# Kernel optimization log

Measured on AMD Instinct MI355X. Metric: run time of the kernel, lower is better.

Reference implementation:

```python
import jax, jax.numpy as jnp
import numpy as np

B, C, H, W, K = 8, 512, 64, 64, 3
EPS = 1e-8


def setup_inputs() -> dict:
    key = jax.random.key(0)
    ks = jax.random.split(key, 7)
    return {
        "x": jax.random.normal(ks[0], (B, C, H, W), jnp.float32),
        "w": jax.random.normal(ks[1], (B, C), jnp.float32),
        "noise": jax.random.normal(ks[2], (B, 1, H, W), jnp.float32),
        # learned params (randn init as in the torch module)
        "conv_weight": jax.random.normal(ks[3], (C, C, K, K), jnp.float32),   # [out_ch, in_ch, k, k]
        "style_weight": jax.random.normal(ks[4], (C, C), jnp.float32),        # EqualizedLinear weight
        "style_bias": jnp.zeros((C,), jnp.float32),
        "bias": jax.random.normal(ks[5], (C,), jnp.float32),
        "scale_noise": jax.random.normal(ks[6], (1,), jnp.float32),
    }


def reference(x, w, noise, conv_weight, style_weight, style_bias, bias, scale_noise):
    b, c, h, wd = x.shape
    c_style = 1.0 / np.sqrt(C)          # EqualizedWeights c for [C, C]
    c_conv = 1.0 / np.sqrt(C * K * K)   # EqualizedWeights c for [C, C, K, K]

    # style vector s: equalized linear
    s = w @ (style_weight * c_style).T + style_bias            # [B, C]

    # per-sample modulation of input channels, demodulation per output channel
    wmod = (conv_weight * c_conv)[None] * s[:, None, :, None, None]   # [B, O, I, K, K]
    demod = jax.lax.rsqrt(jnp.sum(wmod * wmod, axis=(2, 3, 4), keepdims=True) + EPS)
    wmod = wmod * demod

    # grouped conv: fold batch into channels, one group per sample
    xg = x.reshape(1, b * c, h, wd)
    wg = wmod.reshape(b * C, C, K, K)
    y = jax.lax.conv_general_dilated(
        xg, wg, window_strides=(1, 1), padding="SAME",
        feature_group_count=b, dimension_numbers=("NCHW", "OIHW", "NCHW"))
    y = y.reshape(b, C, h, wd)

    # noise + bias + LeakyReLU(0.2)
    y = y + scale_noise[None, :, None, None] * noise
    return jax.nn.leaky_relu(y + bias[None, :, None, None], negative_slope=0.2)
```

## Files before the change

### kernel.cpp

```cpp
#include <hip/hip_runtime.h>


#define CC 512
#define BB 8
#define HWSZ 4096

#define C_STYLE 0.04419417382415922f
#define C_CONV  0.014731391274719739f

typedef __attribute__((ext_vector_type(8))) short bf16x8;
typedef __attribute__((ext_vector_type(4))) float f32x4;

static __device__ __forceinline__ short f2bf(float f) {
  unsigned u = __float_as_uint(f);
  unsigned r = (u + 0x7fffu + ((u >> 16) & 1u)) >> 16;
  return (short)r;
}

static __device__ __forceinline__ void load_lds_16(const void* g, void* l) {
  __builtin_amdgcn_global_load_lds(
      (const __attribute__((address_space(1))) unsigned int*)g,
      (__attribute__((address_space(3))) unsigned int*)l, 16, 0, 0);
}

__global__ void wprep_kernel(const float* __restrict__ cw,
                             short* __restrict__ wfrag,
                             float* __restrict__ wsq) {
  int t0 = blockIdx.x * blockDim.x + threadIdx.x;
  int o = t0 >> 9;
  int i = t0 & 511;
  int ib32 = i >> 5;
  int ob = o >> 4;
  int lane = (o & 15) + (((i >> 3) & 3) << 4);
  int j = i & 7;
  const float* p = cw + (size_t)t0 * 9;
  float s = 0.f;
#pragma unroll
  for (int t = 0; t < 9; ++t) {
    float v = p[t];
    s = fmaf(v, v, s);
    wfrag[((((size_t)t * 16 + ib32) * 32 + ob) * 64 + lane) * 8 + j] = f2bf(v);
  }
  wsq[t0] = s;
}

__global__ void style_alpha_kernel(const float* __restrict__ w,
                                   const float* __restrict__ sw,
                                   const float* __restrict__ sbias,
                                   float* __restrict__ alpha) {
  int wv = (blockIdx.x * blockDim.x + threadIdx.x) >> 6;
  int lane = threadIdx.x & 63;
  int b = wv >> 9;
  int j = wv & 511;
  float acc = 0.f;
  const float* wr = w + b * CC;
  const float* sr = sw + (size_t)j * CC;
#pragma unroll
  for (int k = 0; k < CC; k += 64) acc = fmaf(wr[k + lane], sr[k + lane], acc);
#pragma unroll
  for (int off = 32; off > 0; off >>= 1) acc += __shfl_down(acc, off);
  if (lane == 0) alpha[wv] = C_CONV * fmaf(C_STYLE, acc, sbias[j]);
}

__global__ void demod_kernel(const float* __restrict__ alpha,
                             const float* __restrict__ wsq,
                             float* __restrict__ demod) {
  int wv = (blockIdx.x * blockDim.x + threadIdx.x) >> 6;
  int lane = threadIdx.x & 63;
  int b = wv >> 9;
  int o = wv & 511;
  const float* ar = alpha + b * CC;
  const float* qr = wsq + (size_t)o * CC;
  float s = 0.f;
#pragma unroll
  for (int i = 0; i < CC; i += 64) {
    float a = ar[i + lane];
    s = fmaf(a * a, qr[i + lane], s);
  }
#pragma unroll
  for (int off = 32; off > 0; off >>= 1) s += __shfl_down(s, off);
  if (lane == 0) {
    s += 1e-8f;
    float r = rsqrtf(s);
    r = r * fmaf(-0.5f * s * r, r, 1.5f);
    demod[wv] = r;
  }
}

__global__ void xprep_kernel(const float* __restrict__ x,
                             const float* __restrict__ alpha,
                             short* __restrict__ xT) {
  const int py = blockIdx.x;
  const int ic = blockIdx.y * 4 + (threadIdx.x >> 6);
  const int b = blockIdx.z;
  const int px = threadIdx.x & 63;
  bf16x8 v = (bf16x8){0, 0, 0, 0, 0, 0, 0, 0};
  if (py >= 1 && py <= 64) {
    const float* xp = x + (((size_t)b * CC + ic * 8) * HWSZ + (py - 1) * 64 + px);
    const float* al = alpha + b * CC + ic * 8;
#pragma unroll
    for (int j = 0; j < 8; ++j) v[j] = f2bf(xp[(size_t)j * HWSZ] * al[j]);
  }
  short* row = xT + (((size_t)(b * 64 + ic) * 66 + py) * 66) * 8;
  *(bf16x8*)(row + (px + 1) * 8) = v;
  bf16x8 z = (bf16x8){0, 0, 0, 0, 0, 0, 0, 0};
  if (px == 0) *(bf16x8*)(row) = z;
  if (px == 63) *(bf16x8*)(row + 65 * 8) = z;
}

#define NCHUNK 2112
__global__ __launch_bounds__(256, 2) void conv_kernel(
    const short* __restrict__ xT,
    const short* __restrict__ wfrag,
    const float* __restrict__ noise,
    const float* __restrict__ bias,
    const float* __restrict__ scale_noise,
    const float* __restrict__ demod,
    float* __restrict__ out) {
  __shared__ __align__(16) short xs[2 * NCHUNK * 8];

  const int lin = blockIdx.x + 32 * blockIdx.y + 64 * blockIdx.z;
  const int xcd = lin & 7;
  const int j = lin >> 3;
  const int G = xcd & 1;
  const int b = (xcd >> 1) + 4 * (j & 1);
  const int y0 = (j >> 1) * 2;
  const int tid = threadIdx.x;
  const int lane = tid & 63;
  const int wave = tid >> 6;
  const int n = lane & 15;
  const int quad = lane >> 4;

  f32x4 acc[4][8];
#pragma unroll
  for (int p = 0; p < 4; ++p)
#pragma unroll
    for (int q = 0; q < 8; ++q) acc[p][q] = (f32x4){0.f, 0.f, 0.f, 0.f};

  const char* xTb = (const char*)xT;
  unsigned goff[9];
#pragma unroll
  for (int it = 0; it < 9; ++it) {
    int cid = tid + it * 256;
    int kc = cid / 264;
    int rem = cid - kc * 264;
    int r = rem / 66;
    int c = rem - r * 66;
    goff[it] = (unsigned)((((b * 64 + kc) * 66 + (y0 + r)) * 66 + c) * 16);
  }

  const short* wf0 = wfrag + ((size_t)((G * 16 + wave * 4) * 64 + lane)) * 8;

#pragma unroll
  for (int it = 0; it < 9; ++it) {
    int cid = tid + it * 256;
    if (cid < NCHUNK) load_lds_16(xTb + goff[it], xs + (size_t)cid * 8);
    goff[it] += 8 * 66 * 66 * 16;
  }

  for (int ib = 0; ib < 8; ++ib) {
    const int sel = ib & 1;
    asm volatile("s_waitcnt vmcnt(0)" ::: "memory");
    __builtin_amdgcn_s_barrier();
    if (ib < 7) {
#pragma unroll
      for (int it = 0; it < 9; ++it) {
        int cid = tid + it * 256;
        if (cid < NCHUNK)
          load_lds_16(xTb + goff[it],
                      xs + (size_t)((sel ^ 1) * NCHUNK + cid) * 8);
        goff[it] += 8 * 66 * 66 * 16;
      }
    }
    const short* cxs = xs + (size_t)sel * NCHUNK * 8;

#pragma unroll
    for (int kstep = 0; kstep < 2; ++kstep) {
      const int ib32 = ib * 2 + kstep;
#pragma unroll
      for (int t = 0; t < 9; ++t) {
        const int dy = t / 3 - 1;
        const int dx = t % 3 - 1;
        const short* wp = wf0 + (size_t)(t * 16 + ib32) * 16384;
        bf16x8 af[4];
#pragma unroll
        for (int p = 0; p < 4; ++p)
          af[p] = *(const bf16x8*)(wp + p * 512);
        const short* bp =
            cxs + (((kstep * 4 + quad) * 4 + dy + 1) * 66 + 1 + n + dx) * 8;
        bf16x8 bf[8];
#pragma unroll
        for (int q = 0; q < 8; ++q)
          bf[q] = *(const bf16x8*)(bp + ((q >> 2) * 66 + (q & 3) * 16) * 8);
        __builtin_amdgcn_s_setprio(1);
#pragma unroll
        for (int p = 0; p < 4; ++p)
#pragma unroll
          for (int q = 0; q < 8; ++q)
            acc[p][q] = __builtin_amdgcn_mfma_f32_16x16x32_bf16(
                af[p], bf[q], acc[p][q], 0, 0, 0);
        __builtin_amdgcn_s_setprio(0);
      }
    }
  }

  const float sn = scale_noise[0];
#pragma unroll
  for (int q = 0; q < 8; ++q) {
    const int y = y0 + (q >> 2);
    const int col = (q & 3) * 16 + n;
    const float nz = sn * noise[b * HWSZ + y * 64 + col];
#pragma unroll
    for (int p = 0; p < 4; ++p) {
      const int o0 = G * 256 + wave * 64 + p * 16 + quad * 4;
#pragma unroll
      for (int r = 0; r < 4; ++r) {
        const int o = o0 + r;
        float v = fmaf(acc[p][q][r], demod[b * CC + o], nz + bias[o]);
        out[((size_t)(b * CC + o)) * HWSZ + y * 64 + col] =
            v > 0.f ? v : 0.2f * v;
      }
    }
  }
}

extern "C" void kernel_launch(void* const* d_in, const int* in_sizes, int n_in,
                              void* d_out, int out_size, void* d_ws, size_t ws_size,
                              hipStream_t stream) {
  const float* x     = (const float*)d_in[0];
  const float* w     = (const float*)d_in[1];
  const float* noise = (const float*)d_in[2];
  const float* cw    = (const float*)d_in[3];
  const float* sw    = (const float*)d_in[4];
  const float* sbias = (const float*)d_in[5];
  const float* bias  = (const float*)d_in[6];
  const float* sn    = (const float*)d_in[7];
  float* out = (float*)d_out;

  float* alpha = (float*)d_ws;
  float* demod = alpha + BB * CC;
  float* wsq   = demod + BB * CC;
  short* wfrag = (short*)(wsq + CC * CC);
  short* xT    = wfrag + (size_t)9 * 16 * 32 * 64 * 8;

  style_alpha_kernel<<<dim3(BB * CC / 4), 256, 0, stream>>>(w, sw, sbias, alpha);
  wprep_kernel<<<dim3((CC * CC) / 256), 256, 0, stream>>>(cw, wfrag, wsq);
  demod_kernel<<<dim3(BB * CC / 4), 256, 0, stream>>>(alpha, wsq, demod);
  xprep_kernel<<<dim3(66, 16, BB), 256, 0, stream>>>(x, alpha, xT);
  conv_kernel<<<dim3(32, 2, BB), 256, 0, stream>>>(
      xT, wfrag, noise, bias, sn, demod, out);
}
```

Baseline: 254.7 us.

## Double-buffer weight fragments in registers and defer LDS prefetch to end of K-block

The per-tap loop is flattened into 18 steps. The A (weight) fragments for the next tap are loaded into a second register buffer while the current tap's MFMAs run, and the s_setprio hints are removed. The global-to-LDS prefetch of the next input block moves from the start of the iteration to after the 17th tap, so in-order vmcnt waits on weight loads no longer sit behind the bulk x loads. The cost is that the x prefetch now has only about one tap of compute to hide its latency before the barrier, and the extra fragment buffer raises register pressure.

```diff
diff --git a/kernel.cpp b/kernel.cpp
--- a/kernel.cpp
+++ b/kernel.cpp
@@ -162,44 +162,52 @@
     const int sel = ib & 1;
     asm volatile("s_waitcnt vmcnt(0)" ::: "memory");
     __builtin_amdgcn_s_barrier();
-    if (ib < 7) {
-#pragma unroll
-      for (int it = 0; it < 9; ++it) {
-        int cid = tid + it * 256;
-        if (cid < NCHUNK)
-          load_lds_16(xTb + goff[it],
-                      xs + (size_t)((sel ^ 1) * NCHUNK + cid) * 8);
-        goff[it] += 8 * 66 * 66 * 16;
+    const short* cxs = xs + (size_t)sel * NCHUNK * 8;
+
+    bf16x8 afp[2][4];
+    {
+      const short* wp = wf0 + (size_t)(0 * 16 + ib * 2) * 16384;
+#pragma unroll
+      for (int p = 0; p < 4; ++p) afp[0][p] = *(const bf16x8*)(wp + p * 512);
+    }
+
+#pragma unroll
+    for (int tt = 0; tt < 18; ++tt) {
+      const int cu = tt & 1;
+      const int kstep = tt / 9;
+      const int t = tt - kstep * 9;
+      const int dy = t / 3 - 1;
+      const int dx = t % 3 - 1;
+      if (tt < 17) {
+        const int ks2 = (tt + 1) / 9;
+        const int t2 = (tt + 1) - ks2 * 9;
+        const short* wp2 =
+            wf0 + (size_t)(t2 * 16 + ib * 2 + ks2) * 16384;
+#pragma unroll
+        for (int p = 0; p < 4; ++p)
+          afp[cu ^ 1][p] = *(const bf16x8*)(wp2 + p * 512);
       }
-    }
-    const short* cxs = xs + (size_t)sel * NCHUNK * 8;
-
-#pragma unroll
-    for (int kstep = 0; kstep < 2; ++kstep) {
-      const int ib32 = ib * 2 + kstep;
-#pragma unroll
-      for (int t = 0; t < 9; ++t) {
-        const int dy = t / 3 - 1;
-        const int dx = t % 3 - 1;
-        const short* wp = wf0 + (size_t)(t * 16 + ib32) * 16384;
-        bf16x8 af[4];
-#pragma unroll
-        for (int p = 0; p < 4; ++p)
-          af[p] = *(const bf16x8*)(wp + p * 512);
-        const short* bp =
-            cxs + (((kstep * 4 + quad) * 4 + dy + 1) * 66 + 1 + n + dx) * 8;
-        bf16x8 bf[8];
+      const short* bp =
+          cxs + (((kstep * 4 + quad) * 4 + dy + 1) * 66 + 1 + n + dx) * 8;
+      bf16x8 bfv[8];
+#pragma unroll
+      for (int q = 0; q < 8; ++q)
+        bfv[q] = *(const bf16x8*)(bp + ((q >> 2) * 66 + (q & 3) * 16) * 8);
+#pragma unroll
+      for (int p = 0; p < 4; ++p)
 #pragma unroll
         for (int q = 0; q < 8; ++q)
-          bf[q] = *(const bf16x8*)(bp + ((q >> 2) * 66 + (q & 3) * 16) * 8);
-        __builtin_amdgcn_s_setprio(1);
-#pragma unroll
-        for (int p = 0; p < 4; ++p)
-#pragma unroll
-          for (int q = 0; q < 8; ++q)
-            acc[p][q] = __builtin_amdgcn_mfma_f32_16x16x32_bf16(
-                af[p], bf[q], acc[p][q], 0, 0, 0);
-        __builtin_amdgcn_s_setprio(0);
+          acc[p][q] = __builtin_amdgcn_mfma_f32_16x16x32_bf16(
+              afp[cu][p], bfv[q], acc[p][q], 0, 0, 0);
+      if (tt == 16 && ib < 7) {
+#pragma unroll
+        for (int it = 0; it < 9; ++it) {
+          int cid = tid + it * 256;
+          if (cid < NCHUNK)
+            load_lds_16(xTb + goff[it],
+                        xs + (size_t)((sel ^ 1) * NCHUNK + cid) * 8);
+          goff[it] += 8 * 66 * 66 * 16;
+        }
       }
     }
   }
```

Measured after the change: 287.6 us. 12.9% more time.
